# Performance work log

Measured on AMD Instinct MI355X. Metric: run time of the kernel, lower is better.

## Reference

```python
import jax, jax.numpy as jnp
import numpy as np

H = 16  # hidden_size
IN = 1  # input_size

def setup_inputs() -> dict:
    key = jax.random.key(0)
    ks = jax.random.split(key, 7)
    B, T = 2048, 2048
    s_ih = 1.0 / np.sqrt(H)
    return {
        "x": jax.random.normal(ks[0], (B, T, IN), dtype=jnp.float32),
        # PyTorch LSTM param layout: [4H, in] / [4H, H], gate order i,f,g,o
        "W_ih": jax.random.uniform(ks[1], (4 * H, IN), jnp.float32, -s_ih, s_ih),
        "W_hh": jax.random.uniform(ks[2], (4 * H, H), jnp.float32, -s_ih, s_ih),
        "b_ih": jax.random.uniform(ks[3], (4 * H,), jnp.float32, -s_ih, s_ih),
        "b_hh": jax.random.uniform(ks[4], (4 * H,), jnp.float32, -s_ih, s_ih),
        "W_fc": jax.random.uniform(ks[5], (1, H), jnp.float32, -s_ih, s_ih),
        "b_fc": jax.random.uniform(ks[6], (1,), jnp.float32, -s_ih, s_ih),
    }

def reference(x, W_ih, W_hh, b_ih, b_hh, W_fc, b_fc):
    B = x.shape[0]
    # Precompute input contribution for all timesteps: [T, B, 4H]
    xg = jnp.swapaxes(x, 0, 1) @ W_ih.T + (b_ih + b_hh)

    def step(carry, xt):
        h, c = carry
        g = xt + h @ W_hh.T  # [B, 4H]
        i, f, gg, o = jnp.split(g, 4, axis=-1)  # PyTorch gate order i,f,g,o
        i = jax.nn.sigmoid(i)
        f = jax.nn.sigmoid(f)
        gg = jnp.tanh(gg)
        o = jax.nn.sigmoid(o)
        c = f * c + i * gg
        h = o * jnp.tanh(c)
        return (h, c), None

    h0 = jnp.zeros((B, H), x.dtype)
    (h_last, _), _ = jax.lax.scan(step, (h0, h0), xg)
    # fc applied only to last timestep's hidden state (x[:, -1, :] in torch)
    return h_last @ W_fc.T + b_fc
```

## Files before the change

kernel.cpp:

```cpp
#include <hip/hip_runtime.h>


__device__ __forceinline__ float i2f(int i) { return __int_as_float(i); }
__device__ __forceinline__ int   f2i(float f) { return __float_as_int(f); }

#define LOG2E 1.44269504088896340736f

#define FMAC_DPP(acc, h_, w_, n)                                               \
    asm("v_fmac_f32_dpp %0, %1, %2 row_ror:" #n " row_mask:0xf bank_mask:0xf"  \
        : "+v"(acc) : "v"(h_), "v"(w_));

#define STEP(s_imm) {                                                        \
    float xs_ = i2f(__builtin_amdgcn_readlane(f2i(xblk), (s_imm)));          \
    float aA_ = fmaf(wih_s, xs_, bias_s);                                    \
    aA_ = fmaf(hcur, w[0], aA_);                                             \
    FMAC_DPP(aA_, hcur, w[1], 1)                                             \
    FMAC_DPP(aA_, hcur, w[2], 2)                                             \
    FMAC_DPP(aA_, hcur, w[3], 3)                                             \
    FMAC_DPP(aA_, hcur, w[4], 4)                                             \
    FMAC_DPP(aA_, hcur, w[5], 5)                                             \
    FMAC_DPP(aA_, hcur, w[6], 6)                                             \
    FMAC_DPP(aA_, hcur, w[7], 7)                                             \
    float aB_;                                                               \
    asm("v_mul_f32_dpp %0, %1, %2 row_ror:8 row_mask:0xf bank_mask:0xf"      \
        : "=v"(aB_) : "v"(hcur), "v"(w[8]));                                 \
    FMAC_DPP(aB_, hcur, w[9],  9)                                            \
    FMAC_DPP(aB_, hcur, w[10], 10)                                           \
    FMAC_DPP(aB_, hcur, w[11], 11)                                           \
    FMAC_DPP(aB_, hcur, w[12], 12)                                           \
    FMAC_DPP(aB_, hcur, w[13], 13)                                           \
    FMAC_DPP(aB_, hcur, w[14], 14)                                           \
    FMAC_DPP(aB_, hcur, w[15], 15)                                           \
    float acc_ = aA_ + aB_;                                                  \
    float e_   = __builtin_amdgcn_exp2f(acc_);               \
    float r_   = __builtin_amdgcn_rcpf(1.0f + e_);                           \
    float act_ = fmaf(aco, r_, bco);                                         \
    int   ai_  = f2i(act_);                                                  \
    float gi_  = i2f(__builtin_amdgcn_ds_bpermute(addr_i, ai_));             \
    float gf_  = i2f(__builtin_amdgcn_ds_bpermute(addr_f, ai_));             \
    float gg_  = i2f(__builtin_amdgcn_ds_bpermute(addr_g, ai_));             \
    float go_  = i2f(__builtin_amdgcn_ds_bpermute(addr_o, ai_));             \
    c = fmaf(gf_, c, gi_ * gg_);                \
    float e2_ = __builtin_amdgcn_exp2f(c);                                   \
    float r2_ = __builtin_amdgcn_rcpf(1.0f + e2_);                           \
    float th_ = fmaf(2.0f, r2_, -1.0f);                                      \
    hcur = go_ * th_;                                                        \
}

#define STEP8(base) STEP(base+0) STEP(base+1) STEP(base+2) STEP(base+3) \
                    STEP(base+4) STEP(base+5) STEP(base+6) STEP(base+7)

__global__ __launch_bounds__(256) void lstm_fused(
    const float* __restrict__ x,
    const float* __restrict__ Wih,
    const float* __restrict__ Whh,
    const float* __restrict__ bih,
    const float* __restrict__ bhh,
    const float* __restrict__ Wfc,
    const float* __restrict__ bfc,
    float* __restrict__ out)
{
    const int T   = 2048;
    const int tid = blockIdx.x * blockDim.x + threadIdx.x;
    const int b   = tid >> 6;
    const int l   = threadIdx.x & 63;
    const int j   = l & 15;
    const int gate = l >> 4;

    int probe = __builtin_amdgcn_mov_dpp(j, 0x121, 0xF, 0xF, true);
    const int dir = (probe == ((j + 1) & 15)) ? 1 : -1;

    const float mco = (gate == 2) ? (-2.0f * LOG2E) : (-LOG2E);
    const float aco = (gate == 2) ? (-4.0f * LOG2E) : 1.0f;
    const float bco = (gate == 2) ? ( 2.0f * LOG2E) : 0.0f;

    float w[16];
#pragma unroll
    for (int s = 0; s < 16; ++s) {
        int k = (j + s * dir + 32) & 15;
        w[s] = Whh[l * 16 + k] * mco;
    }

    const float wih_s  = Wih[l] * mco;
    const float bias_s = (bih[l] + bhh[l]) * mco;

    const int addr_i = (j     ) << 2;
    const int addr_f = (j + 16) << 2;
    const int addr_g = (j + 32) << 2;
    const int addr_o = (j + 48) << 2;

    const float* xp = x + (size_t)b * T;
    float xblk = xp[l];

    float hcur = 0.0f, c = 0.0f;

#pragma unroll 1
    for (int blk = 0; blk < 32; ++blk) {
        const int nxt = (blk < 31) ? (blk + 1) : 31;
        float xnext = xp[nxt * 64 + l];
        STEP8(0) STEP8(8) STEP8(16) STEP8(24)
        STEP8(32) STEP8(40) STEP8(48) STEP8(56)
        xblk = xnext;
    }

    float p = hcur * (Wfc[j] * 0.25f);
    p += __shfl_xor(p, 32);
    p += __shfl_xor(p, 16);
    p += __shfl_xor(p, 8);
    p += __shfl_xor(p, 4);
    p += __shfl_xor(p, 2);
    p += __shfl_xor(p, 1);
    if (l == 0) out[b] = p + bfc[0];
}

extern "C" void kernel_launch(void* const* d_in, const int* in_sizes, int n_in,
                              void* d_out, int out_size, void* d_ws, size_t ws_size,
                              hipStream_t stream) {
    const float* x   = (const float*)d_in[0];
    const float* Wih = (const float*)d_in[1];
    const float* Whh = (const float*)d_in[2];
    const float* bih = (const float*)d_in[3];
    const float* bhh = (const float*)d_in[4];
    const float* Wfc = (const float*)d_in[5];
    const float* bfc = (const float*)d_in[6];
    float* out = (float*)d_out;

    const int B = 2048;
    const int threads = 256;
    const int blocks = (B * 64) / threads;
    hipLaunchKernelGGL(lstm_fused, dim3(blocks), dim3(threads), 0, stream,
                       x, Wih, Whh, bih, bhh, Wfc, bfc, out);
}
```

Measured before the change: 402.5 us.

## Replace LDS bpermute gate gather with permlane16/32 swaps and runtime fallback

Gathers the four gate activations across the 16-lane groups with permlane16_swap and permlane32_swap register permutes plus lane-mask selects, instead of four ds_bpermute operations that go through the LDS crossbar. A one-time runtime probe checks that the swap semantics match and otherwise falls back to the original bpermute path. The inner unroll also shrinks from 64 steps to 16 per sub-block with a rolled loop, trading code size for a little loop overhead. The intent is to cut the per-step latency of the serial recurrence. It adds select instructions and three dependent swaps.

```diff
diff --git a/kernel.cpp b/kernel.cpp
--- a/kernel.cpp
+++ b/kernel.cpp
@@ -5,50 +5,109 @@
 __device__ __forceinline__ int   f2i(float f) { return __float_as_int(f); }
 
 #define LOG2E 1.44269504088896340736f
+
+#if __has_builtin(__builtin_amdgcn_permlane16_swap) && __has_builtin(__builtin_amdgcn_permlane32_swap)
+#define HAVE_PERMSWAP 1
+#else
+#define HAVE_PERMSWAP 0
+#endif
+
+typedef unsigned __attribute__((ext_vector_type(2))) uint2v;
 
 #define FMAC_DPP(acc, h_, w_, n)                                               \
     asm("v_fmac_f32_dpp %0, %1, %2 row_ror:" #n " row_mask:0xf bank_mask:0xf"  \
         : "+v"(acc) : "v"(h_), "v"(w_));
-
-#define STEP(s_imm) {                                                        \
-    float xs_ = i2f(__builtin_amdgcn_readlane(f2i(xblk), (s_imm)));          \
-    float aA_ = fmaf(wih_s, xs_, bias_s);                                    \
-    aA_ = fmaf(hcur, w[0], aA_);                                             \
-    FMAC_DPP(aA_, hcur, w[1], 1)                                             \
-    FMAC_DPP(aA_, hcur, w[2], 2)                                             \
-    FMAC_DPP(aA_, hcur, w[3], 3)                                             \
-    FMAC_DPP(aA_, hcur, w[4], 4)                                             \
-    FMAC_DPP(aA_, hcur, w[5], 5)                                             \
-    FMAC_DPP(aA_, hcur, w[6], 6)                                             \
-    FMAC_DPP(aA_, hcur, w[7], 7)                                             \
-    float aB_;                                                               \
-    asm("v_mul_f32_dpp %0, %1, %2 row_ror:8 row_mask:0xf bank_mask:0xf"      \
-        : "=v"(aB_) : "v"(hcur), "v"(w[8]));                                 \
-    FMAC_DPP(aB_, hcur, w[9],  9)                                            \
-    FMAC_DPP(aB_, hcur, w[10], 10)                                           \
-    FMAC_DPP(aB_, hcur, w[11], 11)                                           \
-    FMAC_DPP(aB_, hcur, w[12], 12)                                           \
-    FMAC_DPP(aB_, hcur, w[13], 13)                                           \
-    FMAC_DPP(aB_, hcur, w[14], 14)                                           \
-    FMAC_DPP(aB_, hcur, w[15], 15)                                           \
-    float acc_ = aA_ + aB_;                                                  \
-    float e_   = __builtin_amdgcn_exp2f(acc_);               \
-    float r_   = __builtin_amdgcn_rcpf(1.0f + e_);                           \
-    float act_ = fmaf(aco, r_, bco);                                         \
-    int   ai_  = f2i(act_);                                                  \
-    float gi_  = i2f(__builtin_amdgcn_ds_bpermute(addr_i, ai_));             \
-    float gf_  = i2f(__builtin_amdgcn_ds_bpermute(addr_f, ai_));             \
-    float gg_  = i2f(__builtin_amdgcn_ds_bpermute(addr_g, ai_));             \
-    float go_  = i2f(__builtin_amdgcn_ds_bpermute(addr_o, ai_));             \
-    c = fmaf(gf_, c, gi_ * gg_);                \
-    float e2_ = __builtin_amdgcn_exp2f(c);                                   \
-    float r2_ = __builtin_amdgcn_rcpf(1.0f + e2_);                           \
-    float th_ = fmaf(2.0f, r2_, -1.0f);                                      \
-    hcur = go_ * th_;                                                        \
+#define MUL_DPP(dst, h_, w_, n)                                                \
+    asm("v_mul_f32_dpp %0, %1, %2 row_ror:" #n " row_mask:0xf bank_mask:0xf"   \
+        : "=v"(dst) : "v"(h_), "v"(w_));
+
+template<bool FAST>
+__device__ __forceinline__ float lstm_run(
+    const float* __restrict__ xp, const float (&w)[16],
+    float wih_s, float bias_s, float aco, float bco,
+    bool m16, bool m32, bool b4, bool b5,
+    int a_i, int a_f, int a_g, int a_o, int l)
+{
+    float hcur = 0.0f, c = 0.0f;
+    float xblk = xp[l];
+
+#pragma unroll 1
+    for (int blk = 0; blk < 32; ++blk) {
+        const int nxt = (blk < 31) ? (blk + 1) : 31;
+        float xnext = xp[nxt * 64 + l];
+#pragma unroll 1
+        for (int sub = 0; sub < 4; ++sub) {
+            const int base = sub << 4;
+#pragma unroll
+            for (int k = 0; k < 16; ++k) {
+                float xs = i2f(__builtin_amdgcn_readlane(f2i(xblk), base + k));
+                float aA = fmaf(wih_s, xs, bias_s);
+                aA = fmaf(hcur, w[0], aA);
+                FMAC_DPP(aA, hcur, w[1], 1)
+                FMAC_DPP(aA, hcur, w[2], 2)
+                FMAC_DPP(aA, hcur, w[3], 3)
+                FMAC_DPP(aA, hcur, w[4], 4)
+                FMAC_DPP(aA, hcur, w[5], 5)
+                FMAC_DPP(aA, hcur, w[6], 6)
+                FMAC_DPP(aA, hcur, w[7], 7)
+                float aB;
+                MUL_DPP(aB, hcur, w[8], 8)
+                FMAC_DPP(aB, hcur, w[9],  9)
+                FMAC_DPP(aB, hcur, w[10], 10)
+                FMAC_DPP(aB, hcur, w[11], 11)
+                FMAC_DPP(aB, hcur, w[12], 12)
+                FMAC_DPP(aB, hcur, w[13], 13)
+                FMAC_DPP(aB, hcur, w[14], 14)
+                FMAC_DPP(aB, hcur, w[15], 15)
+                float acc = aA + aB;
+                float e   = __builtin_amdgcn_exp2f(acc);
+                float r   = __builtin_amdgcn_rcpf(1.0f + e);
+                float act = fmaf(aco, r, bco);
+
+                float f_, o_, ig;
+                if constexpr (FAST) {
+#if HAVE_PERMSWAP
+                    uint2v t16 = __builtin_amdgcn_permlane16_swap(
+                        (unsigned)f2i(act), (unsigned)f2i(act), false, false);
+                    float P1 = i2f(m16 ? (int)t16[0] : (int)t16[1]);
+                    uint2v t32 = __builtin_amdgcn_permlane32_swap(
+                        (unsigned)f2i(act), (unsigned)f2i(act), false, false);
+                    float P2 = i2f(m32 ? (int)t32[0] : (int)t32[1]);
+                    uint2v t48 = __builtin_amdgcn_permlane32_swap(
+                        (unsigned)f2i(P1), (unsigned)f2i(P1), false, false);
+                    float P3 = i2f(m32 ? (int)t48[0] : (int)t48[1]);
+                    float u  = b4 ? P1 : act;
+                    float v  = b4 ? P3 : P2;
+                    ig       = u * v;
+                    float fa = b5 ? P3 : P1;
+                    float fb = b5 ? P2 : act;
+                    f_       = b4 ? fb : fa;
+                    float oa = b5 ? P1 : P3;
+                    float ob = b5 ? act : P2;
+                    o_       = b4 ? ob : oa;
+#else
+                    f_ = o_ = ig = 0.0f;
+#endif
+                } else {
+                    int ai = f2i(act);
+                    float gi = i2f(__builtin_amdgcn_ds_bpermute(a_i, ai));
+                    float gf = i2f(__builtin_amdgcn_ds_bpermute(a_f, ai));
+                    float gg = i2f(__builtin_amdgcn_ds_bpermute(a_g, ai));
+                    float go = i2f(__builtin_amdgcn_ds_bpermute(a_o, ai));
+                    f_ = gf; o_ = go; ig = gi * gg;
+                }
+
+                c = fmaf(f_, c, ig);
+                float e2 = __builtin_amdgcn_exp2f(c);
+                float r2 = __builtin_amdgcn_rcpf(1.0f + e2);
+                float th = fmaf(2.0f, r2, -1.0f);
+                hcur = o_ * th;
+            }
+        }
+        xblk = xnext;
+    }
+    return hcur;
 }
-
-#define STEP8(base) STEP(base+0) STEP(base+1) STEP(base+2) STEP(base+3) \
-                    STEP(base+4) STEP(base+5) STEP(base+6) STEP(base+7)
 
 __global__ __launch_bounds__(256) void lstm_fused(
     const float* __restrict__ x,
@@ -66,6 +125,8 @@
     const int l   = threadIdx.x & 63;
     const int j   = l & 15;
     const int gate = l >> 4;
+    const bool b4 = (l >> 4) & 1;
+    const bool b5 = (l >> 5) & 1;
 
     int probe = __builtin_amdgcn_mov_dpp(j, 0x121, 0xF, 0xF, true);
     const int dir = (probe == ((j + 1) & 15)) ? 1 : -1;
@@ -77,31 +138,42 @@
     float w[16];
 #pragma unroll
     for (int s = 0; s < 16; ++s) {
-        int k = (j + s * dir + 32) & 15;
-        w[s] = Whh[l * 16 + k] * mco;
+        int kk = (j + s * dir + 32) & 15;
+        w[s] = Whh[l * 16 + kk] * mco;
     }
-
     const float wih_s  = Wih[l] * mco;
     const float bias_s = (bih[l] + bhh[l]) * mco;
 
-    const int addr_i = (j     ) << 2;
-    const int addr_f = (j + 16) << 2;
-    const int addr_g = (j + 32) << 2;
-    const int addr_o = (j + 48) << 2;
+    const int a_i = (j     ) << 2;
+    const int a_f = (j + 16) << 2;
+    const int a_g = (j + 32) << 2;
+    const int a_o = (j + 48) << 2;
+
+    bool fast = false, m16 = false, m32 = false;
+#if HAVE_PERMSWAP
+    {
+        uint2v p = __builtin_amdgcn_permlane16_swap((unsigned)l, (unsigned)l,
+                                                    false, false);
+        int want16 = l ^ 16;
+        m16 = ((int)p[0] == want16);
+        int got16 = m16 ? (int)p[0] : (int)p[1];
+        uint2v q = __builtin_amdgcn_permlane32_swap((unsigned)l, (unsigned)l,
+                                                    false, false);
+        int want32 = l ^ 32;
+        m32 = ((int)q[0] == want32);
+        int got32 = m32 ? (int)q[0] : (int)q[1];
+        fast = __all(got16 == want16) && __all(got32 == want32);
+    }
+#endif
 
     const float* xp = x + (size_t)b * T;
-    float xblk = xp[l];
-
-    float hcur = 0.0f, c = 0.0f;
-
-#pragma unroll 1
-    for (int blk = 0; blk < 32; ++blk) {
-        const int nxt = (blk < 31) ? (blk + 1) : 31;
-        float xnext = xp[nxt * 64 + l];
-        STEP8(0) STEP8(8) STEP8(16) STEP8(24)
-        STEP8(32) STEP8(40) STEP8(48) STEP8(56)
-        xblk = xnext;
-    }
+    float hcur;
+    if (fast)
+        hcur = lstm_run<true >(xp, w, wih_s, bias_s, aco, bco, m16, m32, b4, b5,
+                               a_i, a_f, a_g, a_o, l);
+    else
+        hcur = lstm_run<false>(xp, w, wih_s, bias_s, aco, bco, m16, m32, b4, b5,
+                               a_i, a_f, a_g, a_o, l);
 
     float p = hcur * (Wfc[j] * 0.25f);
     p += __shfl_xor(p, 32);
```

Result: slower. 479.3 us (+19.1%).

## Pack four batch rows per wave with all gates computed per lane

Applied to the files above, without the earlier changes.

Changes the mapping so each 16-lane row handles one batch element and each lane computes all four gates (i,f,g,o) for its hidden unit. This removes the per-step ds_bpermute gate exchange and replaces x broadcast via readlane with ds_swizzle. Each wave now serves four sequences instead of one, using 4x fewer waves with 64 weight registers per lane. The cost is four times more FMAs per lane per step and much higher register pressure, while cross-lane latency on the recurrent critical path drops.

```diff
diff --git a/kernel.cpp b/kernel.cpp
--- a/kernel.cpp
+++ b/kernel.cpp
@@ -10,47 +10,42 @@
     asm("v_fmac_f32_dpp %0, %1, %2 row_ror:" #n " row_mask:0xf bank_mask:0xf"  \
         : "+v"(acc) : "v"(h_), "v"(w_));
 
-#define STEP(s_imm) {                                                        \
-    float xs_ = i2f(__builtin_amdgcn_readlane(f2i(xblk), (s_imm)));          \
-    float aA_ = fmaf(wih_s, xs_, bias_s);                                    \
-    aA_ = fmaf(hcur, w[0], aA_);                                             \
-    FMAC_DPP(aA_, hcur, w[1], 1)                                             \
-    FMAC_DPP(aA_, hcur, w[2], 2)                                             \
-    FMAC_DPP(aA_, hcur, w[3], 3)                                             \
-    FMAC_DPP(aA_, hcur, w[4], 4)                                             \
-    FMAC_DPP(aA_, hcur, w[5], 5)                                             \
-    FMAC_DPP(aA_, hcur, w[6], 6)                                             \
-    FMAC_DPP(aA_, hcur, w[7], 7)                                             \
-    float aB_;                                                               \
-    asm("v_mul_f32_dpp %0, %1, %2 row_ror:8 row_mask:0xf bank_mask:0xf"      \
-        : "=v"(aB_) : "v"(hcur), "v"(w[8]));                                 \
-    FMAC_DPP(aB_, hcur, w[9],  9)                                            \
-    FMAC_DPP(aB_, hcur, w[10], 10)                                           \
-    FMAC_DPP(aB_, hcur, w[11], 11)                                           \
-    FMAC_DPP(aB_, hcur, w[12], 12)                                           \
-    FMAC_DPP(aB_, hcur, w[13], 13)                                           \
-    FMAC_DPP(aB_, hcur, w[14], 14)                                           \
-    FMAC_DPP(aB_, hcur, w[15], 15)                                           \
-    float acc_ = aA_ + aB_;                                                  \
-    float e_   = __builtin_amdgcn_exp2f(acc_);               \
-    float r_   = __builtin_amdgcn_rcpf(1.0f + e_);                           \
-    float act_ = fmaf(aco, r_, bco);                                         \
-    int   ai_  = f2i(act_);                                                  \
-    float gi_  = i2f(__builtin_amdgcn_ds_bpermute(addr_i, ai_));             \
-    float gf_  = i2f(__builtin_amdgcn_ds_bpermute(addr_f, ai_));             \
-    float gg_  = i2f(__builtin_amdgcn_ds_bpermute(addr_g, ai_));             \
-    float go_  = i2f(__builtin_amdgcn_ds_bpermute(addr_o, ai_));             \
-    c = fmaf(gf_, c, gi_ * gg_);                \
-    float e2_ = __builtin_amdgcn_exp2f(c);                                   \
-    float r2_ = __builtin_amdgcn_rcpf(1.0f + e2_);                           \
-    float th_ = fmaf(2.0f, r2_, -1.0f);                                      \
-    hcur = go_ * th_;                                                        \
+#define ROT4(s)                                                              \
+    FMAC_DPP(a0_, h, w0[s], s) FMAC_DPP(a1_, h, w1[s], s)                    \
+    FMAC_DPP(a2_, h, w2[s], s) FMAC_DPP(a3_, h, w3[s], s)
+
+#define STEP(K) {                                                            \
+    float xc_ = i2f(__builtin_amdgcn_ds_swizzle(f2i(xblk),                   \
+                                                (((K) << 5) | 0x10)));       \
+    float a0_ = fmaf(wi0, xc_, bs0);                                         \
+    float a1_ = fmaf(wi1, xc_, bs1);                                         \
+    float a2_ = fmaf(wi2, xc_, bs2);                                         \
+    float a3_ = fmaf(wi3, xc_, bs3);                                         \
+    a0_ = fmaf(h, w0[0], a0_);                                               \
+    a1_ = fmaf(h, w1[0], a1_);                                               \
+    a2_ = fmaf(h, w2[0], a2_);                                               \
+    a3_ = fmaf(h, w3[0], a3_);                                               \
+    ROT4(1)  ROT4(2)  ROT4(3)  ROT4(4)  ROT4(5)  ROT4(6)  ROT4(7)            \
+    ROT4(8)  ROT4(9)  ROT4(10) ROT4(11) ROT4(12) ROT4(13) ROT4(14) ROT4(15)  \
+    float e0_  = __builtin_amdgcn_exp2f(a0_);                                \
+    float e1_  = __builtin_amdgcn_exp2f(a1_);                                \
+    float e2_  = __builtin_amdgcn_exp2f(a2_);                                \
+    float e3_  = __builtin_amdgcn_exp2f(a3_);                                \
+    float ri_  = __builtin_amdgcn_rcpf(1.0f + e0_);            \
+    float rf_  = __builtin_amdgcn_rcpf(1.0f + e1_);            \
+    float rg_  = __builtin_amdgcn_rcpf(1.0f + e2_);                          \
+    float ro_  = __builtin_amdgcn_rcpf(1.0f + e3_);            \
+    float gs_  = fmaf(-4.0f * LOG2E, rg_, 2.0f * LOG2E);   \
+    c = fmaf(rf_, c, ri_ * gs_);                    \
+    float ec_  = __builtin_amdgcn_exp2f(c);                                  \
+    float rc_  = __builtin_amdgcn_rcpf(1.0f + ec_);                          \
+    float o2_  = ro_ + ro_;                                   \
+    h = fmaf(o2_, rc_, -ro_);                               \
 }
 
-#define STEP8(base) STEP(base+0) STEP(base+1) STEP(base+2) STEP(base+3) \
-                    STEP(base+4) STEP(base+5) STEP(base+6) STEP(base+7)
-
-__global__ __launch_bounds__(256) void lstm_fused(
+__global__ __launch_bounds__(64, 1)
+__attribute__((amdgpu_waves_per_eu(1)))
+void lstm_fused(
     const float* __restrict__ x,
     const float* __restrict__ Wih,
     const float* __restrict__ Whh,
@@ -61,56 +56,55 @@
     float* __restrict__ out)
 {
     const int T   = 2048;
-    const int tid = blockIdx.x * blockDim.x + threadIdx.x;
-    const int b   = tid >> 6;
-    const int l   = threadIdx.x & 63;
+    const int l   = threadIdx.x;
+    const int row = l >> 4;
     const int j   = l & 15;
-    const int gate = l >> 4;
+    const int b   = blockIdx.x * 4 + row;
 
     int probe = __builtin_amdgcn_mov_dpp(j, 0x121, 0xF, 0xF, true);
     const int dir = (probe == ((j + 1) & 15)) ? 1 : -1;
 
-    const float mco = (gate == 2) ? (-2.0f * LOG2E) : (-LOG2E);
-    const float aco = (gate == 2) ? (-4.0f * LOG2E) : 1.0f;
-    const float bco = (gate == 2) ? ( 2.0f * LOG2E) : 0.0f;
-
-    float w[16];
+    const int r0 = (0  + j) * 16, r1 = (16 + j) * 16,
+              r2 = (32 + j) * 16, r3 = (48 + j) * 16;
+    float w0[16], w1[16], w2[16], w3[16];
 #pragma unroll
     for (int s = 0; s < 16; ++s) {
         int k = (j + s * dir + 32) & 15;
-        w[s] = Whh[l * 16 + k] * mco;
+        w0[s] = Whh[r0 + k] * (-LOG2E);
+        w1[s] = Whh[r1 + k] * (-LOG2E);
+        w2[s] = Whh[r2 + k] * (-2.0f * LOG2E);
+        w3[s] = Whh[r3 + k] * (-LOG2E);
+    }
+    const float wi0 = Wih[ 0 + j] * (-LOG2E);
+    const float wi1 = Wih[16 + j] * (-LOG2E);
+    const float wi2 = Wih[32 + j] * (-2.0f * LOG2E);
+    const float wi3 = Wih[48 + j] * (-LOG2E);
+    const float bs0 = (bih[ 0 + j] + bhh[ 0 + j]) * (-LOG2E);
+    const float bs1 = (bih[16 + j] + bhh[16 + j]) * (-LOG2E);
+    const float bs2 = (bih[32 + j] + bhh[32 + j]) * (-2.0f * LOG2E);
+    const float bs3 = (bih[48 + j] + bhh[48 + j]) * (-LOG2E);
+
+    const float* xp = x + (size_t)b * T;
+    float xblk = xp[j];
+    float h = 0.0f, c = 0.0f;
+
+#pragma unroll 1
+    for (int blk = 0; blk < 128; ++blk) {
+        const int nxt = (blk < 127) ? blk + 1 : 127;
+        float xn = xp[nxt * 16 + j];
+        STEP(0)  STEP(1)  STEP(2)  STEP(3)
+        STEP(4)  STEP(5)  STEP(6)  STEP(7)
+        STEP(8)  STEP(9)  STEP(10) STEP(11)
+        STEP(12) STEP(13) STEP(14) STEP(15)
+        xblk = xn;
     }
 
-    const float wih_s  = Wih[l] * mco;
-    const float bias_s = (bih[l] + bhh[l]) * mco;
-
-    const int addr_i = (j     ) << 2;
-    const int addr_f = (j + 16) << 2;
-    const int addr_g = (j + 32) << 2;
-    const int addr_o = (j + 48) << 2;
-
-    const float* xp = x + (size_t)b * T;
-    float xblk = xp[l];
-
-    float hcur = 0.0f, c = 0.0f;
-
-#pragma unroll 1
-    for (int blk = 0; blk < 32; ++blk) {
-        const int nxt = (blk < 31) ? (blk + 1) : 31;
-        float xnext = xp[nxt * 64 + l];
-        STEP8(0) STEP8(8) STEP8(16) STEP8(24)
-        STEP8(32) STEP8(40) STEP8(48) STEP8(56)
-        xblk = xnext;
-    }
-
-    float p = hcur * (Wfc[j] * 0.25f);
-    p += __shfl_xor(p, 32);
-    p += __shfl_xor(p, 16);
+    float p = h * Wfc[j];
+    p += __shfl_xor(p, 1);
+    p += __shfl_xor(p, 2);
+    p += __shfl_xor(p, 4);
     p += __shfl_xor(p, 8);
-    p += __shfl_xor(p, 4);
-    p += __shfl_xor(p, 2);
-    p += __shfl_xor(p, 1);
-    if (l == 0) out[b] = p + bfc[0];
+    if (j == 0) out[b] = p + bfc[0];
 }
 
 extern "C" void kernel_launch(void* const* d_in, const int* in_sizes, int n_in,
@@ -126,8 +120,8 @@
     float* out = (float*)d_out;
 
     const int B = 2048;
-    const int threads = 256;
-    const int blocks = (B * 64) / threads;
+    const int threads = 64;
+    const int blocks  = B / 4;
     hipLaunchKernelGGL(lstm_fused, dim3(blocks), dim3(threads), 0, stream,
                        x, Wih, Whh, bih, bhh, Wfc, bfc, out);
 }
```

Result: slower. 493.4 us (+22.6%).
